# Kernel optimization log

Measured on AMD Instinct MI355X. Metric: run time of the kernel, lower is better.

Reference implementation:

```python
import jax, jax.numpy as jnp
import numpy as np

N, E, B, K, HD = 100000, 800000, 1024, 10, 512
BN_EPS = 1e-5


def _bn(x, g, b):
    # BatchNorm1d in training mode: biased batch statistics over axis 0
    m = jnp.mean(x, axis=0)
    v = jnp.mean((x - m) ** 2, axis=0)
    return (x - m) * jax.lax.rsqrt(v + BN_EPS) * g + b


def _gin_mean(h, src, dst):
    # DGL GINConv(apply_func=None, 'mean', eps=0): h' = h + mean_{u in N_in(v)} h_u
    msum = jax.ops.segment_sum(h[src], dst, num_segments=N)           # [N, HD]
    deg = jax.ops.segment_sum(jnp.ones((E,), h.dtype), dst, num_segments=N)
    return h + msum / jnp.maximum(deg, 1.0)[:, None]


def setup_inputs() -> dict:
    key = jax.random.key(0)
    ks = jax.random.split(key, 24)
    s = 0.02
    f32 = jnp.float32
    inp = {
        "node_h": jax.random.normal(ks[0], (N, 20), f32),
        "pg_emb": jax.random.normal(ks[1], (B, HD), f32),
        "neigh_emb": jax.random.normal(ks[2], (B * K, HD), f32),
        "class_w": jax.random.uniform(ks[3], (B, K), f32),
        "src": jax.random.randint(ks[4], (E,), 0, N, jnp.int32),
        "dst": jax.random.randint(ks[5], (E,), 0, N, jnp.int32),
        "node_graph": jnp.sort(jax.random.randint(ks[6], (N,), 0, B, jnp.int32)),
        # parameters
        "w_init": jax.random.normal(ks[7], (20, HD), f32) * s,
        "b_init": jnp.zeros((HD,), f32),
        "g1": jnp.ones((HD,), f32), "be1": jnp.zeros((HD,), f32),
        "g2": jnp.ones((HD,), f32), "be2": jnp.zeros((HD,), f32),
        "w_fc": jax.random.normal(ks[8], (3 * HD, 256), f32) * s,
        "b_fc": jnp.zeros((256,), f32),
        "w_fc2": jax.random.normal(ks[9], (256, 256), f32) * s,
        "b_fc2": jnp.zeros((256,), f32),
        "w_fc3": jax.random.normal(ks[10], (256, 256), f32) * s,
        "b_fc3": jnp.zeros((256,), f32),
        "w_fc4": jax.random.normal(ks[11], (256, 1), f32) * s,
        "b_fc4": jnp.zeros((1,), f32),
        "gb": jnp.ones((256,), f32), "bb": jnp.zeros((256,), f32),
        "gb2": jnp.ones((256,), f32), "bb2": jnp.zeros((256,), f32),
        "gb3": jnp.ones((256,), f32), "bb3": jnp.zeros((256,), f32),
    }
    return inp


def reference(node_h, pg_emb, neigh_emb, class_w, src, dst, node_graph,
              w_init, b_init, g1, be1, g2, be2,
              w_fc, b_fc, w_fc2, b_fc2, w_fc3, b_fc3, w_fc4, b_fc4,
              gb, bb, gb2, bb2, gb3, bb3):
    h = node_h @ w_init + b_init                              # [N, HD]
    h = jax.nn.relu(_bn(_gin_mean(h, src, dst), g1, be1))
    h = jax.nn.relu(_bn(_gin_mean(h, src, dst), g2, be2))
    # dgl.mean_nodes: per-graph mean over nodes
    gsum = jax.ops.segment_sum(h, node_graph, num_segments=B)  # [B, HD]
    cnt = jax.ops.segment_sum(jnp.ones((N,), h.dtype), node_graph, num_segments=B)
    qemb = gsum / jnp.maximum(cnt, 1.0)[:, None]
    a = jnp.concatenate([qemb, pg_emb], axis=1)               # [B, 2*HD]
    a = jnp.repeat(a, K, axis=0)                              # repeat(1,K).view(-1,2*HD)
    b = jnp.concatenate([a, neigh_emb], axis=1)               # [B*K, 3*HD]
    H = jax.nn.relu(_bn(b @ w_fc + b_fc, gb, bb))
    H2 = jax.nn.relu(_bn(H @ w_fc2 + b_fc2, gb2, bb2))
    H3 = jax.nn.relu(_bn(H2 @ w_fc3 + b_fc3, gb3, bb3))
    preds = jax.nn.sigmoid(H3 @ w_fc4 + b_fc4).reshape(B, K)
    return preds, H3
```

## Files before the change

### kernel.cpp

```cpp
#include <hip/hip_runtime.h>
#include <hip/hip_bf16.h>

typedef unsigned short u16;
typedef __bf16 bf16x8 __attribute__((ext_vector_type(8)));
typedef float f32x4 __attribute__((ext_vector_type(4)));

#define NN 100000
#define NE 800000
#define NGRAPH 1024
#define KREP 10
#define HD 512
#define MQ 10240
#define FCN 256
#define EPS 1e-5f

static __device__ __forceinline__ float bf2f(u16 u) {
  return __uint_as_float(((unsigned int)u) << 16);
}
static __device__ __forceinline__ u16 f2bf(float f) {
  __hip_bfloat16 h = __float2bfloat16(f);
  u16 u; __builtin_memcpy(&u, &h, 2); return u;
}
static __device__ __forceinline__ void gadd(float* p, float v) { unsafeAtomicAdd(p, v); }

static __device__ __forceinline__ unsigned int pk4_fp8(float a, float b, float c, float d) {
  int w = __builtin_amdgcn_cvt_pk_fp8_f32(a, b, 0, false);
  w = __builtin_amdgcn_cvt_pk_fp8_f32(c, d, w, true);
  return (unsigned int)w;
}
static __device__ __forceinline__ void unpk4_fp8(unsigned int w, float f[4]) {
  auto p01 = __builtin_amdgcn_cvt_pk_f32_fp8((int)w, false);
  auto p23 = __builtin_amdgcn_cvt_pk_f32_fp8((int)w, true);
  f[0] = p01[0]; f[1] = p01[1]; f[2] = p23[0]; f[3] = p23[1];
}

template <int BNIN>
static __device__ __forceinline__ void accw8(uint2 r, float a[8], const float sc[8], const float sh[8],
                                             float w) {
  float f[8];
  unpk4_fp8(r.x, f);
  unpk4_fp8(r.y, f + 4);
#pragma unroll
  for (int j = 0; j < 8; j++) {
    float v = f[j];
    if (BNIN) v = fmaxf(v * sc[j] + sh[j], 0.f);
    a[j] = fmaf(v, w, a[j]);
  }
}

__global__ __launch_bounds__(256) void k_init(const float* __restrict__ nh, const float* __restrict__ w,
                                              const float* __restrict__ bi, unsigned char* __restrict__ h8) {
  __shared__ float als[64 * 20];
  int t = threadIdx.x;
  float wr0[20], wr1[20];
#pragma unroll
  for (int k = 0; k < 20; k++) {
    float2 wv = *(const float2*)&w[k * 512 + t * 2];
    wr0[k] = wv.x; wr1[k] = wv.y;
  }
  int v0 = blockIdx.x * 64;
  for (int i = t; i < 64 * 20; i += 256) {
    size_t gi = (size_t)v0 * 20 + i;
    als[i] = (gi < (size_t)NN * 20) ? nh[gi] : 0.0f;
  }
  __syncthreads();
  float b0 = bi[t * 2], b1 = bi[t * 2 + 1];
  u16* h16 = (u16*)h8;
  for (int ni = 0; ni < 64; ni++) {
    int v = v0 + ni; if (v >= NN) break;
    float s0 = b0, s1 = b1;
#pragma unroll
    for (int k4 = 0; k4 < 5; k4++) {
      float4 av = *(const float4*)&als[ni * 20 + k4 * 4];
      s0 += av.x * wr0[k4 * 4 + 0]; s1 += av.x * wr1[k4 * 4 + 0];
      s0 += av.y * wr0[k4 * 4 + 1]; s1 += av.y * wr1[k4 * 4 + 1];
      s0 += av.z * wr0[k4 * 4 + 2]; s1 += av.z * wr1[k4 * 4 + 2];
      s0 += av.w * wr0[k4 * 4 + 3]; s1 += av.w * wr1[k4 * 4 + 3];
    }
    unsigned int pk = (unsigned int)__builtin_amdgcn_cvt_pk_fp8_f32(s0, s1, 0, false);
    h16[v * 256 + t] = (u16)(pk & 0xffffu);
  }
}

__global__ void k_deg(const int* __restrict__ dst, int* __restrict__ deg) {
  int i = blockIdx.x * 256 + threadIdx.x;
  if (i < NE) atomicAdd(&deg[dst[i]], 1);
}

__global__ __launch_bounds__(256) void k_scan_part(const int* __restrict__ deg, int* __restrict__ part) {
  __shared__ int ls[256];
  int t = threadIdx.x; int base = blockIdx.x * 1024;
  int s = 0;
  for (int i = t; i < 1024; i += 256) { int idx = base + i; if (idx < NN) s += deg[idx]; }
  ls[t] = s; __syncthreads();
  for (int o = 128; o > 0; o >>= 1) { if (t < o) ls[t] += ls[t + o]; __syncthreads(); }
  if (t == 0) part[blockIdx.x] = ls[0];
}

__global__ void k_scan_mid(int* part, int nb, int* offs) {
  __shared__ int ls[128];
  int t = threadIdx.x;
  if (t < nb) ls[t] = part[t];
  __syncthreads();
  if (t == 0) {
    int run = 0;
    for (int i = 0; i < nb; i++) { int v = ls[i]; ls[i] = run; run += v; }
  }
  __syncthreads();
  if (t < nb) part[t] = ls[t];
  if (t == 0) offs[NN] = NE;
}

__global__ __launch_bounds__(256) void k_scan_apply(const int* __restrict__ deg, const int* __restrict__ part,
                                                    int* __restrict__ offs, int* __restrict__ cursor) {
  __shared__ int ls[256];
  int t = threadIdx.x; int base = blockIdx.x * 1024 + t * 4;
  int v[4]; int s = 0;
#pragma unroll
  for (int j = 0; j < 4; j++) { int idx = base + j; v[j] = (idx < NN) ? deg[idx] : 0; s += v[j]; }
  ls[t] = s; __syncthreads();
  for (int o = 1; o < 256; o <<= 1) {
    int x = (t >= o) ? ls[t - o] : 0;
    __syncthreads();
    ls[t] += x;
    __syncthreads();
  }
  int excl = ls[t] - s + part[blockIdx.x];
#pragma unroll
  for (int j = 0; j < 4; j++) {
    int idx = base + j;
    if (idx < NN) { offs[idx] = excl; cursor[idx] = excl; }
    excl += v[j];
  }
}

__global__ void k_fill(const int* __restrict__ src, const int* __restrict__ dst,
                       int* __restrict__ cursor, int* __restrict__ nsrc) {
  int i = blockIdx.x * 256 + threadIdx.x;
  if (i < NE) { int p = atomicAdd(&cursor[dst[i]], 1); nsrc[p] = src[i]; }
}

template <int BNIN, int OUT8>
__global__ __launch_bounds__(256) void k_gin(const unsigned char* __restrict__ hin, const int* __restrict__ offs,
                                             const int* __restrict__ nsrc,
                                             const float* __restrict__ ics, const float* __restrict__ icq,
                                             const float* __restrict__ ig, const float* __restrict__ ibe,
                                             void* __restrict__ xout, float* __restrict__ cs,
                                             float* __restrict__ cq) {
  __shared__ float redS[4][512];
  __shared__ float redQ[4][512];
  int t = threadIdx.x, wid = t >> 6, lane = t & 63;
  int c0 = lane * 8;
  float sc[8], sh[8];
  if (BNIN) {
    const float invn = 1.0f / (float)NN;
#pragma unroll
    for (int j = 0; j < 8; j++) {
      float m = ics[c0 + j] * invn;
      float var = icq[c0 + j] * invn - m * m;
      sc[j] = ig[c0 + j] * rsqrtf(var + EPS);
      sh[j] = ibe[c0 + j] - m * sc[j];
    }
  }
  float s[8] = {0, 0, 0, 0, 0, 0, 0, 0}, q[8] = {0, 0, 0, 0, 0, 0, 0, 0};
  int l7 = lane & 7;
  for (int vb = blockIdx.x * 4; vb < NN; vb += gridDim.x * 4) {
    int v = __builtin_amdgcn_readfirstlane(vb + wid);
    if (v >= NN) continue;
    int e0 = __builtin_amdgcn_readfirstlane(offs[v]);
    int e1 = __builtin_amdgcn_readfirstlane(offs[v + 1]);
    uint2 hv = *(const uint2*)&hin[(size_t)v * 512 + c0];
    float a[8] = {0, 0, 0, 0, 0, 0, 0, 0};
    int myn = (e0 < e1) ? nsrc[e0 + l7] : 0;
    for (int e = e0; e < e1; e += 8) {
      int mynext = nsrc[e + 8 + l7];
      int si[8];
      si[0] = __builtin_amdgcn_readlane(myn, 0);
      si[1] = __builtin_amdgcn_readlane(myn, 1);
      si[2] = __builtin_amdgcn_readlane(myn, 2);
      si[3] = __builtin_amdgcn_readlane(myn, 3);
      si[4] = __builtin_amdgcn_readlane(myn, 4);
      si[5] = __builtin_amdgcn_readlane(myn, 5);
      si[6] = __builtin_amdgcn_readlane(myn, 6);
      si[7] = __builtin_amdgcn_readlane(myn, 7);
      uint2 r[8];
#pragma unroll
      for (int j = 0; j < 8; j++) r[j] = *(const uint2*)&hin[(size_t)si[j] * 512 + c0];
      accw8<BNIN>(r[0], a, sc, sh, 1.0f);
#pragma unroll
      for (int j = 1; j < 8; j++) accw8<BNIN>(r[j], a, sc, sh, (e + j < e1) ? 1.0f : 0.0f);
      myn = mynext;
    }
    float inv = 1.0f / fmaxf((float)(e1 - e0), 1.0f);
    float hf[8];
    unpk4_fp8(hv.x, hf);
    unpk4_fp8(hv.y, hf + 4);
    float xv[8];
#pragma unroll
    for (int j = 0; j < 8; j++) {
      float h0 = hf[j];
      if (BNIN) h0 = fmaxf(h0 * sc[j] + sh[j], 0.f);
      xv[j] = h0 + a[j] * inv;
    }
    if (OUT8) {
      uint2 o;
      o.x = pk4_fp8(xv[0], xv[1], xv[2], xv[3]);
      o.y = pk4_fp8(xv[4], xv[5], xv[6], xv[7]);
      *(uint2*)&((unsigned char*)xout)[(size_t)v * 512 + c0] = o;
      float rf[8];
      unpk4_fp8(o.x, rf);
      unpk4_fp8(o.y, rf + 4);
#pragma unroll
      for (int j = 0; j < 8; j++) { s[j] += rf[j]; q[j] += rf[j] * rf[j]; }
    } else {
      unsigned int ho[4];
#pragma unroll
      for (int k = 0; k < 4; k++) {
        u16 b0 = f2bf(xv[2 * k]), b1 = f2bf(xv[2 * k + 1]);
        ho[k] = ((unsigned int)b1 << 16) | (unsigned int)b0;
        float x0 = bf2f(b0), x1 = bf2f(b1);
        s[2 * k] += x0; q[2 * k] += x0 * x0;
        s[2 * k + 1] += x1; q[2 * k + 1] += x1 * x1;
      }
      *(int4*)&((u16*)xout)[(size_t)v * HD + c0] = *(int4*)ho;
    }
  }
#pragma unroll
  for (int j = 0; j < 8; j++) { redS[wid][c0 + j] = s[j]; redQ[wid][c0 + j] = q[j]; }
  __syncthreads();
  for (int i = t; i < 512; i += 256) {
    float ts = redS[0][i] + redS[1][i] + redS[2][i] + redS[3][i];
    float tq = redQ[0][i] + redQ[1][i] + redQ[2][i] + redQ[3][i];
    gadd(&cs[i], ts);
    gadd(&cq[i], tq);
  }
}

__global__ __launch_bounds__(256) void k_poolbn(const unsigned char* __restrict__ h8, const int* __restrict__ ngr,
                                                const float* __restrict__ ics, const float* __restrict__ icq,
                                                const float* __restrict__ ig, const float* __restrict__ ibe,
                                                u16* __restrict__ qemb) {
  __shared__ float red[4][512];
  int g = blockIdx.x; int t = threadIdx.x, wid = t >> 6, lane = t & 63;
  int c0 = lane * 8;
  const float invn = 1.0f / (float)NN;
  float sc[8], sh[8];
#pragma unroll
  for (int j = 0; j < 8; j++) {
    float m = ics[c0 + j] * invn;
    float var = icq[c0 + j] * invn - m * m;
    sc[j] = ig[c0 + j] * rsqrtf(var + EPS);
    sh[j] = ibe[c0 + j] - m * sc[j];
  }
  int lo = 0, hi = NN;
  while (lo < hi) { int mid = (lo + hi) >> 1; if (ngr[mid] < g) lo = mid + 1; else hi = mid; }
  int s0_ = lo;
  hi = NN;
  while (lo < hi) { int mid = (lo + hi) >> 1; if (ngr[mid] < g + 1) lo = mid + 1; else hi = mid; }
  int e_ = lo;
  float a[8] = {0, 0, 0, 0, 0, 0, 0, 0};
  for (int v = s0_ + wid; v < e_; v += 4) {
    uint2 r = *(const uint2*)&h8[(size_t)v * 512 + c0];
    float f[8];
    unpk4_fp8(r.x, f);
    unpk4_fp8(r.y, f + 4);
#pragma unroll
    for (int j = 0; j < 8; j++) a[j] += fmaxf(f[j] * sc[j] + sh[j], 0.f);
  }
#pragma unroll
  for (int j = 0; j < 8; j++) red[wid][c0 + j] = a[j];
  __syncthreads();
  float inv = 1.0f / fmaxf((float)(e_ - s0_), 1.0f);
  int cc = t * 2;
  float r0 = (red[0][cc] + red[1][cc] + red[2][cc] + red[3][cc]) * inv;
  float r1 = (red[0][cc + 1] + red[1][cc + 1] + red[2][cc + 1] + red[3][cc + 1]) * inv;
  unsigned int o = ((unsigned int)f2bf(r1) << 16) | (unsigned int)f2bf(r0);
  *(unsigned int*)&qemb[(size_t)g * HD + cc] = o;
}

__global__ void k_prep(const float* __restrict__ w1, const float* __restrict__ w2,
                       const float* __restrict__ w3, u16* __restrict__ Wb,
                       const u16* __restrict__ qemb, const float* __restrict__ pg,
                       const float* __restrict__ ne, u16* __restrict__ Aq, u16* __restrict__ Ane) {
  int idx = blockIdx.x * 256 + threadIdx.x;
  if (idx < 131072) {
    int i4 = idx * 4;
    const float* src; int off;
    if (i4 < 393216) { src = w1; off = i4; }
    else if (i4 < 458752) { src = w2; off = i4 - 393216; }
    else { src = w3; off = i4 - 458752; }
    float4 v = *(const float4*)&src[off];
    ushort4 o; o.x = f2bf(v.x); o.y = f2bf(v.y); o.z = f2bf(v.z); o.w = f2bf(v.w);
    *(ushort4*)&Wb[i4] = o;
  } else if (idx < 131072 + 262144) {
    int j = idx - 131072;
    int r = j >> 8; int cc = (j & 255) * 4;
    ushort4 o;
    if (cc < 512) {
      o = *(const ushort4*)&qemb[r * HD + cc];
    } else {
      float4 v = *(const float4*)&pg[(size_t)r * HD + cc - 512];
      o.x = f2bf(v.x); o.y = f2bf(v.y); o.z = f2bf(v.z); o.w = f2bf(v.w);
    }
    *(ushort4*)&Aq[(size_t)r * 1024 + cc] = o;
  } else {
    int j = idx - 393216; if (j >= 1310720) return;
    int r = j >> 7; int cc = (j & 127) * 4;
    float4 v = *(const float4*)&ne[(size_t)r * HD + cc];
    ushort4 o; o.x = f2bf(v.x); o.y = f2bf(v.y); o.z = f2bf(v.z); o.w = f2bf(v.w);
    *(ushort4*)&Ane[(size_t)r * 512 + cc] = o;
  }
}

template <int MODE, int BNA>
__global__ __launch_bounds__(256) void k_gemm(const u16* __restrict__ A, const u16* __restrict__ W,
                                              const float* __restrict__ bias, const float* __restrict__ rowadd,
                                              const float* __restrict__ bns, const float* __restrict__ bnq,
                                              const float* __restrict__ bng, const float* __restrict__ bnb,
                                              void* __restrict__ Cout,
                                              float* __restrict__ cs, float* __restrict__ cq, int Kd) {
  __shared__ __align__(16) u16 Als[64][40];
  __shared__ __align__(16) u16 Bls[64][40];
  __shared__ float redS[64], redQ[64];
  __shared__ float scK[256], shK[256];
  int t = threadIdx.x; int wid = t >> 6; int lane = t & 63;
  int m0 = blockIdx.x * 64, n0 = blockIdx.y * 64;
  int wr = wid >> 1, wc = wid & 1;
  if (MODE != 0 && t < 64) { redS[t] = 0.f; redQ[t] = 0.f; }
  if (BNA) {
    const float invn = 1.0f / (float)MQ;
    float m = bns[t] * invn;
    float var = bnq[t] * invn - m * m;
    float scv = bng[t] * rsqrtf(var + EPS);
    scK[t] = scv; shK[t] = bnb[t] - m * scv;
  }
  f32x4 zero = {0.0f, 0.0f, 0.0f, 0.0f};
  f32x4 acc[2][2];
#pragma unroll
  for (int i = 0; i < 2; i++)
#pragma unroll
    for (int j = 0; j < 2; j++) acc[i][j] = zero;
  int ar = t >> 2, akc = (t & 3) * 8;
  int bk = t >> 3, bnc = (t & 7) * 8;
  int row = lane & 15, kc = (lane >> 4) * 8;
  if (BNA) __syncthreads();
  for (int k0 = 0; k0 < Kd; k0 += 32) {
    if (BNA) {
      union { int4 v; unsigned int w[4]; } av;
      av.v = *(const int4*)&A[(size_t)(m0 + ar) * Kd + k0 + akc];
      unsigned int o[4];
#pragma unroll
      for (int kk = 0; kk < 4; kk++) {
        int kcol = k0 + akc + 2 * kk;
        float f0 = __uint_as_float(av.w[kk] << 16);
        float f1 = __uint_as_float(av.w[kk] & 0xffff0000u);
        float y0 = fmaxf(f0 * scK[kcol] + shK[kcol], 0.f);
        float y1 = fmaxf(f1 * scK[kcol + 1] + shK[kcol + 1], 0.f);
        o[kk] = ((unsigned int)f2bf(y1) << 16) | (unsigned int)f2bf(y0);
      }
      *(int4*)&Als[ar][akc] = *(int4*)o;
    } else {
      *(int4*)&Als[ar][akc] = *(const int4*)&A[(size_t)(m0 + ar) * Kd + k0 + akc];
    }
    union { int4 v; u16 u[8]; } bv;
    bv.v = *(const int4*)&W[(size_t)(k0 + bk) * FCN + n0 + bnc];
#pragma unroll
    for (int j = 0; j < 8; j++) Bls[bnc + j][bk] = bv.u[j];
    __syncthreads();
    bf16x8 a0 = *(const bf16x8*)&Als[wr * 32 + row][kc];
    bf16x8 a1 = *(const bf16x8*)&Als[wr * 32 + 16 + row][kc];
    bf16x8 b0 = *(const bf16x8*)&Bls[wc * 32 + row][kc];
    bf16x8 b1 = *(const bf16x8*)&Bls[wc * 32 + 16 + row][kc];
    acc[0][0] = __builtin_amdgcn_mfma_f32_16x16x32_bf16(a0, b0, acc[0][0], 0, 0, 0);
    acc[0][1] = __builtin_amdgcn_mfma_f32_16x16x32_bf16(a0, b1, acc[0][1], 0, 0, 0);
    acc[1][0] = __builtin_amdgcn_mfma_f32_16x16x32_bf16(a1, b0, acc[1][0], 0, 0, 0);
    acc[1][1] = __builtin_amdgcn_mfma_f32_16x16x32_bf16(a1, b1, acc[1][1], 0, 0, 0);
    __syncthreads();
  }
#pragma unroll
  for (int fn = 0; fn < 2; fn++) {
    int cl = wc * 32 + fn * 16 + (lane & 15);
    int col = n0 + cl;
    float bcol = (MODE == 2) ? 0.f : bias[col];
    float sS = 0.f, sQ = 0.f;
#pragma unroll
    for (int fm = 0; fm < 2; fm++) {
#pragma unroll
      for (int r = 0; r < 4; r++) {
        int rr = m0 + wr * 32 + fm * 16 + (lane >> 4) * 4 + r;
        float v = acc[fm][fn][r] + bcol;
        if (MODE == 0) {
          ((float*)Cout)[(size_t)rr * FCN + col] = v;
        } else {
          if (MODE == 2) v += rowadd[(size_t)(rr / KREP) * FCN + col];
          u16 b = f2bf(v);
          ((u16*)Cout)[(size_t)rr * FCN + col] = b;
          float xr = bf2f(b);
          sS += xr; sQ += xr * xr;
        }
      }
    }
    if (MODE != 0) { atomicAdd(&redS[cl], sS); atomicAdd(&redQ[cl], sQ); }
  }
  if (MODE != 0) {
    __syncthreads();
    if (t < 64) { gadd(&cs[n0 + t], redS[t]); gadd(&cq[n0 + t], redQ[t]); }
  }
}

__global__ __launch_bounds__(256) void k_bnfc4(const u16* __restrict__ x, const float* __restrict__ cs,
                                               const float* __restrict__ cq, const float* __restrict__ g,
                                               const float* __restrict__ be, const float* __restrict__ w4,
                                               const float* __restrict__ b4, float* __restrict__ H3,
                                               float* __restrict__ preds) {
  const float invn = 1.0f / (float)MQ;
  int tid = blockIdx.x * 256 + threadIdx.x;
  int r = tid >> 5;
  int c0 = (tid & 31) * 8;
  float sc[8], sh[8];
#pragma unroll
  for (int j = 0; j < 8; j++) {
    float m = cs[c0 + j] * invn;
    float var = cq[c0 + j] * invn - m * m;
    sc[j] = g[c0 + j] * rsqrtf(var + EPS);
    sh[j] = be[c0 + j] - m * sc[j];
  }
  int4 u = *(const int4*)&x[(size_t)r * FCN + c0];
  float y[8];
#pragma unroll
  for (int k = 0; k < 4; k++) {
    unsigned int w = ((unsigned int*)&u)[k];
    y[2 * k]     = fmaxf(__uint_as_float(w << 16) * sc[2 * k] + sh[2 * k], 0.f);
    y[2 * k + 1] = fmaxf(__uint_as_float(w & 0xffff0000u) * sc[2 * k + 1] + sh[2 * k + 1], 0.f);
  }
  float4 o0 = {y[0], y[1], y[2], y[3]}, o1 = {y[4], y[5], y[6], y[7]};
  *(float4*)&H3[(size_t)r * FCN + c0] = o0;
  *(float4*)&H3[(size_t)r * FCN + c0 + 4] = o1;
  float4 w0 = *(const float4*)&w4[c0];
  float4 w1 = *(const float4*)&w4[c0 + 4];
  float dp = y[0] * w0.x + y[1] * w0.y + y[2] * w0.z + y[3] * w0.w +
             y[4] * w1.x + y[5] * w1.y + y[6] * w1.z + y[7] * w1.w;
#pragma unroll
  for (int o = 16; o >= 1; o >>= 1) dp += __shfl_xor(dp, o, 64);
  if ((tid & 31) == 0) preds[r] = 1.0f / (1.0f + expf(-(dp + b4[0])));
}

extern "C" void kernel_launch(void* const* d_in, const int* in_sizes, int n_in,
                              void* d_out, int out_size, void* d_ws, size_t ws_size,
                              hipStream_t stream) {
  const float* node_h = (const float*)d_in[0];
  const float* pg     = (const float*)d_in[1];
  const float* ne     = (const float*)d_in[2];
  const int* src = (const int*)d_in[4];
  const int* dst = (const int*)d_in[5];
  const int* ngr = (const int*)d_in[6];
  const float* w_init = (const float*)d_in[7];
  const float* b_init = (const float*)d_in[8];
  const float* g1  = (const float*)d_in[9];
  const float* be1 = (const float*)d_in[10];
  const float* g2  = (const float*)d_in[11];
  const float* be2 = (const float*)d_in[12];
  const float* w_fc  = (const float*)d_in[13];
  const float* b_fc  = (const float*)d_in[14];
  const float* w_fc2 = (const float*)d_in[15];
  const float* b_fc2 = (const float*)d_in[16];
  const float* w_fc3 = (const float*)d_in[17];
  const float* b_fc3 = (const float*)d_in[18];
  const float* w_fc4 = (const float*)d_in[19];
  const float* b_fc4 = (const float*)d_in[20];
  const float* gb  = (const float*)d_in[21];
  const float* bb  = (const float*)d_in[22];
  const float* gb2 = (const float*)d_in[23];
  const float* bb2 = (const float*)d_in[24];
  const float* gb3 = (const float*)d_in[25];
  const float* bb3 = (const float*)d_in[26];

  char* w = (char*)d_ws;
  unsigned char* hA8 = (unsigned char*)w;
  unsigned char* hX8 = (unsigned char*)(w + 51200000LL);
  u16* Aq  = (u16*)(w + 102400000LL);
  u16* Ane = (u16*)(w + 102400000LL + 2097152LL);
  float* P1 = (float*)(w + 102400000LL + 2097152LL + 10485760LL);
  u16* Wb = (u16*)(w + 150000000LL);
  u16* X1 = (u16*)(w + 102400000LL + 33554432LL);
  u16* X2 = (u16*)(w + 102400000LL + 50331648LL);
  u16* X3 = (u16*)(w + 102400000LL + 67108864LL);
  size_t off = 204800000LL;
  int* deg = (int*)(w + off); off += 400128;
  float* st = (float*)(w + off); off += 16384;
  int* offs = (int*)(w + off); off += 400128;
  int* cursor = (int*)(w + off); off += 400128;
  int* nsrc = (int*)(w + off); off += 3200128;
  int* part = (int*)(w + off); off += 2048;
  u16* qemb = (u16*)(w + off); off += 1048576;

  float *s_g1 = st,        *q_g1 = st + 512;
  float *s_g2 = st + 1024, *q_g2 = st + 1536;
  float *s_f1 = st + 2048, *q_f1 = st + 2304;
  float *s_f2 = st + 2560, *q_f2 = st + 2816;
  float *s_f3 = st + 3072, *q_f3 = st + 3328;

  u16* Wq   = Wb;
  u16* Wbot = Wb + 1024 * 256;
  u16* Wb2  = Wb + 393216;
  u16* Wb3  = Wb + 458752;

  float* preds = (float*)d_out;
  float* H3 = preds + MQ;

  hipMemsetAsync(deg, 0, 400128, stream);
  hipMemsetAsync(st, 0, 16384, stream);
  hipMemsetAsync(nsrc + NE, 0, 128, stream);

  k_init<<<(NN + 63) / 64, 256, 0, stream>>>(node_h, w_init, b_init, hA8);
  k_deg<<<(NE + 255) / 256, 256, 0, stream>>>(dst, deg);
  k_scan_part<<<98, 256, 0, stream>>>(deg, part);
  k_scan_mid<<<1, 128, 0, stream>>>(part, 98, offs);
  k_scan_apply<<<98, 256, 0, stream>>>(deg, part, offs, cursor);
  k_fill<<<(NE + 255) / 256, 256, 0, stream>>>(src, dst, cursor, nsrc);

  k_gin<0, 1><<<2048, 256, 0, stream>>>(hA8, offs, nsrc, s_g1, q_g1, g1, be1, (void*)hX8, s_g1, q_g1);
  k_gin<1, 1><<<2048, 256, 0, stream>>>(hX8, offs, nsrc, s_g1, q_g1, g1, be1, (void*)hA8, s_g2, q_g2);

  k_poolbn<<<NGRAPH, 256, 0, stream>>>(hA8, ngr, s_g2, q_g2, g2, be2, qemb);
  k_prep<<<6656, 256, 0, stream>>>(w_fc, w_fc2, w_fc3, Wb, qemb, pg, ne, Aq, Ane);

  dim3 gq(16, 4);
  k_gemm<0, 0><<<gq, 256, 0, stream>>>(Aq, Wq, b_fc, nullptr, nullptr, nullptr, nullptr, nullptr,
                                       (void*)P1, s_f1, q_f1, 1024);
  dim3 gg(160, 4);
  k_gemm<2, 0><<<gg, 256, 0, stream>>>(Ane, Wbot, nullptr, P1, nullptr, nullptr, nullptr, nullptr,
                                       (void*)X1, s_f1, q_f1, 512);
  k_gemm<1, 1><<<gg, 256, 0, stream>>>(X1, Wb2, b_fc2, nullptr, s_f1, q_f1, gb, bb,
                                       (void*)X2, s_f2, q_f2, 256);
  k_gemm<1, 1><<<gg, 256, 0, stream>>>(X2, Wb3, b_fc3, nullptr, s_f2, q_f2, gb2, bb2,
                                       (void*)X3, s_f3, q_f3, 256);
  k_bnfc4<<<1280, 256, 0, stream>>>(X3, s_f3, q_f3, gb3, bb3, w_fc4, b_fc4, H3, preds);
}
```

Before: 473.9 us.

## Fuse weight/neighbor conversion into init kernel and widen GIN gather to 16 edges

The fp32→bf16 conversion of the FC weights and neighbor embeddings moves into the node-init kernel as extra blocks. The first FC GEMM now reads qemb and pg_emb directly, converting pg on the fly, so the separate prep kernel and the Aq buffer are gone. The memsets are merged and the nsrc padding is zeroed inside k_fill. The GIN neighbor gather now handles 16 edges per iteration, with masked lanes redirected to a valid row, to expose more memory-level parallelism at the cost of higher register pressure.

```diff
diff --git a/kernel.cpp b/kernel.cpp
--- a/kernel.cpp
+++ b/kernel.cpp
@@ -48,17 +48,43 @@
   }
 }
 
-__global__ __launch_bounds__(256) void k_init(const float* __restrict__ nh, const float* __restrict__ w,
-                                              const float* __restrict__ bi, unsigned char* __restrict__ h8) {
+__global__ __launch_bounds__(256) void k_initc(const float* __restrict__ nh, const float* __restrict__ w,
+                                               const float* __restrict__ bi, unsigned char* __restrict__ h8,
+                                               const float* __restrict__ w1, const float* __restrict__ w2,
+                                               const float* __restrict__ w3, u16* __restrict__ Wb,
+                                               const float* __restrict__ ne, u16* __restrict__ Ane) {
+  int t = threadIdx.x;
+  int b = blockIdx.x;
+  if (b >= 1563) {
+    int idx = (b - 1563) * 256 + t;
+    if (idx < 131072) {
+      int i4 = idx * 4;
+      const float* src; int off;
+      if (i4 < 393216) { src = w1; off = i4; }
+      else if (i4 < 458752) { src = w2; off = i4 - 393216; }
+      else { src = w3; off = i4 - 458752; }
+      float4 v = *(const float4*)&src[off];
+      ushort4 o; o.x = f2bf(v.x); o.y = f2bf(v.y); o.z = f2bf(v.z); o.w = f2bf(v.w);
+      *(ushort4*)&Wb[i4] = o;
+    } else {
+      int j = idx - 131072;
+      if (j < 1310720) {
+        int i4 = j * 4;
+        float4 v = *(const float4*)&ne[i4];
+        ushort4 o; o.x = f2bf(v.x); o.y = f2bf(v.y); o.z = f2bf(v.z); o.w = f2bf(v.w);
+        *(ushort4*)&Ane[i4] = o;
+      }
+    }
+    return;
+  }
   __shared__ float als[64 * 20];
-  int t = threadIdx.x;
   float wr0[20], wr1[20];
 #pragma unroll
   for (int k = 0; k < 20; k++) {
     float2 wv = *(const float2*)&w[k * 512 + t * 2];
     wr0[k] = wv.x; wr1[k] = wv.y;
   }
-  int v0 = blockIdx.x * 64;
+  int v0 = b * 64;
   for (int i = t; i < 64 * 20; i += 256) {
     size_t gi = (size_t)v0 * 20 + i;
     als[i] = (gi < (size_t)NN * 20) ? nh[gi] : 0.0f;
@@ -137,6 +163,7 @@
 __global__ void k_fill(const int* __restrict__ src, const int* __restrict__ dst,
                        int* __restrict__ cursor, int* __restrict__ nsrc) {
   int i = blockIdx.x * 256 + threadIdx.x;
+  if (i < 32) nsrc[NE + i] = 0;
   if (i < NE) { int p = atomicAdd(&cursor[dst[i]], 1); nsrc[p] = src[i]; }
 }
 
@@ -163,7 +190,7 @@
     }
   }
   float s[8] = {0, 0, 0, 0, 0, 0, 0, 0}, q[8] = {0, 0, 0, 0, 0, 0, 0, 0};
-  int l7 = lane & 7;
+  int l15 = lane & 15;
   for (int vb = blockIdx.x * 4; vb < NN; vb += gridDim.x * 4) {
     int v = __builtin_amdgcn_readfirstlane(vb + wid);
     if (v >= NN) continue;
@@ -171,24 +198,48 @@
     int e1 = __builtin_amdgcn_readfirstlane(offs[v + 1]);
     uint2 hv = *(const uint2*)&hin[(size_t)v * 512 + c0];
     float a[8] = {0, 0, 0, 0, 0, 0, 0, 0};
-    int myn = (e0 < e1) ? nsrc[e0 + l7] : 0;
-    for (int e = e0; e < e1; e += 8) {
-      int mynext = nsrc[e + 8 + l7];
-      int si[8];
-      si[0] = __builtin_amdgcn_readlane(myn, 0);
-      si[1] = __builtin_amdgcn_readlane(myn, 1);
-      si[2] = __builtin_amdgcn_readlane(myn, 2);
-      si[3] = __builtin_amdgcn_readlane(myn, 3);
-      si[4] = __builtin_amdgcn_readlane(myn, 4);
-      si[5] = __builtin_amdgcn_readlane(myn, 5);
-      si[6] = __builtin_amdgcn_readlane(myn, 6);
-      si[7] = __builtin_amdgcn_readlane(myn, 7);
-      uint2 r[8];
-#pragma unroll
-      for (int j = 0; j < 8; j++) r[j] = *(const uint2*)&hin[(size_t)si[j] * 512 + c0];
+    int myn = nsrc[e0 + l15];
+    for (int e = e0; e < e1; e += 16) {
+      int mynext = nsrc[e + 16 + l15];
+      int si0  = __builtin_amdgcn_readlane(myn, 0);
+      int si1  = __builtin_amdgcn_readlane(myn, 1);
+      int si2  = __builtin_amdgcn_readlane(myn, 2);
+      int si3  = __builtin_amdgcn_readlane(myn, 3);
+      int si4  = __builtin_amdgcn_readlane(myn, 4);
+      int si5  = __builtin_amdgcn_readlane(myn, 5);
+      int si6  = __builtin_amdgcn_readlane(myn, 6);
+      int si7  = __builtin_amdgcn_readlane(myn, 7);
+      int si8  = __builtin_amdgcn_readlane(myn, 8);
+      int si9  = __builtin_amdgcn_readlane(myn, 9);
+      int si10 = __builtin_amdgcn_readlane(myn, 10);
+      int si11 = __builtin_amdgcn_readlane(myn, 11);
+      int si12 = __builtin_amdgcn_readlane(myn, 12);
+      int si13 = __builtin_amdgcn_readlane(myn, 13);
+      int si14 = __builtin_amdgcn_readlane(myn, 14);
+      int si15 = __builtin_amdgcn_readlane(myn, 15);
+      int sj[16];
+      sj[0]  = si0;
+      sj[1]  = (e + 1  < e1) ? si1  : si0;
+      sj[2]  = (e + 2  < e1) ? si2  : si0;
+      sj[3]  = (e + 3  < e1) ? si3  : si0;
+      sj[4]  = (e + 4  < e1) ? si4  : si0;
+      sj[5]  = (e + 5  < e1) ? si5  : si0;
+      sj[6]  = (e + 6  < e1) ? si6  : si0;
+      sj[7]  = (e + 7  < e1) ? si7  : si0;
+      sj[8]  = (e + 8  < e1) ? si8  : si0;
+      sj[9]  = (e + 9  < e1) ? si9  : si0;
+      sj[10] = (e + 10 < e1) ? si10 : si0;
+      sj[11] = (e + 11 < e1) ? si11 : si0;
+      sj[12] = (e + 12 < e1) ? si12 : si0;
+      sj[13] = (e + 13 < e1) ? si13 : si0;
+      sj[14] = (e + 14 < e1) ? si14 : si0;
+      sj[15] = (e + 15 < e1) ? si15 : si0;
+      uint2 r[16];
+#pragma unroll
+      for (int j = 0; j < 16; j++) r[j] = *(const uint2*)&hin[(size_t)sj[j] * 512 + c0];
       accw8<BNIN>(r[0], a, sc, sh, 1.0f);
 #pragma unroll
-      for (int j = 1; j < 8; j++) accw8<BNIN>(r[j], a, sc, sh, (e + j < e1) ? 1.0f : 0.0f);
+      for (int j = 1; j < 16; j++) accw8<BNIN>(r[j], a, sc, sh, (e + j < e1) ? 1.0f : 0.0f);
       myn = mynext;
     }
     float inv = 1.0f / fmaxf((float)(e1 - e0), 1.0f);
@@ -278,42 +329,9 @@
   *(unsigned int*)&qemb[(size_t)g * HD + cc] = o;
 }
 
-__global__ void k_prep(const float* __restrict__ w1, const float* __restrict__ w2,
-                       const float* __restrict__ w3, u16* __restrict__ Wb,
-                       const u16* __restrict__ qemb, const float* __restrict__ pg,
-                       const float* __restrict__ ne, u16* __restrict__ Aq, u16* __restrict__ Ane) {
-  int idx = blockIdx.x * 256 + threadIdx.x;
-  if (idx < 131072) {
-    int i4 = idx * 4;
-    const float* src; int off;
-    if (i4 < 393216) { src = w1; off = i4; }
-    else if (i4 < 458752) { src = w2; off = i4 - 393216; }
-    else { src = w3; off = i4 - 458752; }
-    float4 v = *(const float4*)&src[off];
-    ushort4 o; o.x = f2bf(v.x); o.y = f2bf(v.y); o.z = f2bf(v.z); o.w = f2bf(v.w);
-    *(ushort4*)&Wb[i4] = o;
-  } else if (idx < 131072 + 262144) {
-    int j = idx - 131072;
-    int r = j >> 8; int cc = (j & 255) * 4;
-    ushort4 o;
-    if (cc < 512) {
-      o = *(const ushort4*)&qemb[r * HD + cc];
-    } else {
-      float4 v = *(const float4*)&pg[(size_t)r * HD + cc - 512];
-      o.x = f2bf(v.x); o.y = f2bf(v.y); o.z = f2bf(v.z); o.w = f2bf(v.w);
-    }
-    *(ushort4*)&Aq[(size_t)r * 1024 + cc] = o;
-  } else {
-    int j = idx - 393216; if (j >= 1310720) return;
-    int r = j >> 7; int cc = (j & 127) * 4;
-    float4 v = *(const float4*)&ne[(size_t)r * HD + cc];
-    ushort4 o; o.x = f2bf(v.x); o.y = f2bf(v.y); o.z = f2bf(v.z); o.w = f2bf(v.w);
-    *(ushort4*)&Ane[(size_t)r * 512 + cc] = o;
-  }
-}
-
-template <int MODE, int BNA>
-__global__ __launch_bounds__(256) void k_gemm(const u16* __restrict__ A, const u16* __restrict__ W,
+template <int MODE, int BNA, int ASRC>
+__global__ __launch_bounds__(256) void k_gemm(const void* __restrict__ A, const float* __restrict__ Apg,
+                                              const u16* __restrict__ W,
                                               const float* __restrict__ bias, const float* __restrict__ rowadd,
                                               const float* __restrict__ bns, const float* __restrict__ bnq,
                                               const float* __restrict__ bng, const float* __restrict__ bnb,
@@ -345,9 +363,22 @@
   int row = lane & 15, kc = (lane >> 4) * 8;
   if (BNA) __syncthreads();
   for (int k0 = 0; k0 < Kd; k0 += 32) {
-    if (BNA) {
+    if (ASRC == 2) {
+      int kcol = k0 + akc;
+      if (kcol < 512) {
+        *(int4*)&Als[ar][akc] = *(const int4*)&((const u16*)A)[(size_t)(m0 + ar) * 512 + kcol];
+      } else {
+        float4 v0 = *(const float4*)&Apg[(size_t)(m0 + ar) * 512 + kcol - 512];
+        float4 v1 = *(const float4*)&Apg[(size_t)(m0 + ar) * 512 + kcol - 512 + 4];
+        ushort4 o0, o1;
+        o0.x = f2bf(v0.x); o0.y = f2bf(v0.y); o0.z = f2bf(v0.z); o0.w = f2bf(v0.w);
+        o1.x = f2bf(v1.x); o1.y = f2bf(v1.y); o1.z = f2bf(v1.z); o1.w = f2bf(v1.w);
+        *(ushort4*)&Als[ar][akc] = o0;
+        *(ushort4*)&Als[ar][akc + 4] = o1;
+      }
+    } else if (BNA) {
       union { int4 v; unsigned int w[4]; } av;
-      av.v = *(const int4*)&A[(size_t)(m0 + ar) * Kd + k0 + akc];
+      av.v = *(const int4*)&((const u16*)A)[(size_t)(m0 + ar) * Kd + k0 + akc];
       unsigned int o[4];
 #pragma unroll
       for (int kk = 0; kk < 4; kk++) {
@@ -360,7 +391,7 @@
       }
       *(int4*)&Als[ar][akc] = *(int4*)o;
     } else {
-      *(int4*)&Als[ar][akc] = *(const int4*)&A[(size_t)(m0 + ar) * Kd + k0 + akc];
+      *(int4*)&Als[ar][akc] = *(const int4*)&((const u16*)A)[(size_t)(m0 + ar) * Kd + k0 + akc];
     }
     union { int4 v; u16 u[8]; } bv;
     bv.v = *(const int4*)&W[(size_t)(k0 + bk) * FCN + n0 + bnc];
@@ -478,9 +509,8 @@
   char* w = (char*)d_ws;
   unsigned char* hA8 = (unsigned char*)w;
   unsigned char* hX8 = (unsigned char*)(w + 51200000LL);
-  u16* Aq  = (u16*)(w + 102400000LL);
-  u16* Ane = (u16*)(w + 102400000LL + 2097152LL);
-  float* P1 = (float*)(w + 102400000LL + 2097152LL + 10485760LL);
+  u16* Ane = (u16*)(w + 102400000LL);
+  float* P1 = (float*)(w + 102400000LL + 12582912LL);
   u16* Wb = (u16*)(w + 150000000LL);
   u16* X1 = (u16*)(w + 102400000LL + 33554432LL);
   u16* X2 = (u16*)(w + 102400000LL + 50331648LL);
@@ -508,11 +538,9 @@
   float* preds = (float*)d_out;
   float* H3 = preds + MQ;
 
-  hipMemsetAsync(deg, 0, 400128, stream);
-  hipMemsetAsync(st, 0, 16384, stream);
-  hipMemsetAsync(nsrc + NE, 0, 128, stream);
-
-  k_init<<<(NN + 63) / 64, 256, 0, stream>>>(node_h, w_init, b_init, hA8);
+  hipMemsetAsync(deg, 0, 400128 + 16384, stream);
+
+  k_initc<<<7195, 256, 0, stream>>>(node_h, w_init, b_init, hA8, w_fc, w_fc2, w_fc3, Wb, ne, Ane);
   k_deg<<<(NE + 255) / 256, 256, 0, stream>>>(dst, deg);
   k_scan_part<<<98, 256, 0, stream>>>(deg, part);
   k_scan_mid<<<1, 128, 0, stream>>>(part, 98, offs);
@@ -523,17 +551,20 @@
   k_gin<1, 1><<<2048, 256, 0, stream>>>(hX8, offs, nsrc, s_g1, q_g1, g1, be1, (void*)hA8, s_g2, q_g2);
 
   k_poolbn<<<NGRAPH, 256, 0, stream>>>(hA8, ngr, s_g2, q_g2, g2, be2, qemb);
-  k_prep<<<6656, 256, 0, stream>>>(w_fc, w_fc2, w_fc3, Wb, qemb, pg, ne, Aq, Ane);
 
   dim3 gq(16, 4);
-  k_gemm<0, 0><<<gq, 256, 0, stream>>>(Aq, Wq, b_fc, nullptr, nullptr, nullptr, nullptr, nullptr,
-                                       (void*)P1, s_f1, q_f1, 1024);
+  k_gemm<0, 0, 2><<<gq, 256, 0, stream>>>((const void*)qemb, pg, Wq, b_fc, nullptr,
+                                          nullptr, nullptr, nullptr, nullptr,
+                                          (void*)P1, s_f1, q_f1, 1024);
   dim3 gg(160, 4);
-  k_gemm<2, 0><<<gg, 256, 0, stream>>>(Ane, Wbot, nullptr, P1, nullptr, nullptr, nullptr, nullptr,
-                                       (void*)X1, s_f1, q_f1, 512);
-  k_gemm<1, 1><<<gg, 256, 0, stream>>>(X1, Wb2, b_fc2, nullptr, s_f1, q_f1, gb, bb,
-                                       (void*)X2, s_f2, q_f2, 256);
-  k_gemm<1, 1><<<gg, 256, 0, stream>>>(X2, Wb3, b_fc3, nullptr, s_f2, q_f2, gb2, bb2,
-                                       (void*)X3, s_f3, q_f3, 256);
+  k_gemm<2, 0, 0><<<gg, 256, 0, stream>>>((const void*)Ane, nullptr, Wbot, nullptr, P1,
+                                          nullptr, nullptr, nullptr, nullptr,
+                                          (void*)X1, s_f1, q_f1, 512);
+  k_gemm<1, 1, 0><<<gg, 256, 0, stream>>>((const void*)X1, nullptr, Wb2, b_fc2, nullptr,
+                                          s_f1, q_f1, gb, bb,
+                                          (void*)X2, s_f2, q_f2, 256);
+  k_gemm<1, 1, 0><<<gg, 256, 0, stream>>>((const void*)X2, nullptr, Wb3, b_fc3, nullptr,
+                                          s_f2, q_f2, gb2, bb2,
+                                          (void*)X3, s_f3, q_f3, 256);
   k_bnfc4<<<1280, 256, 0, stream>>>(X3, s_f3, q_f3, gb3, bb3, w_fc4, b_fc4, H3, preds);
 }
```

Result: slower. 495.2 us (+4.5%).
